# Kernel tuning notes

Measured on AMD Instinct MI355X. Metric: run time of the kernel, lower is better.

## Reference

```python
import jax, jax.numpy as jnp
import numpy as np

B, F, P, CIN, C, NH, HID, DEPTH = 32, 243, 17, 2, 128, 8, 256, 4
EPS = 1e-6


def setup_inputs() -> dict:
    key = jax.random.key(0)
    ks = jax.random.split(key, 9)
    s = jnp.float32(0.02)
    return {
        "x": jax.random.normal(ks[0], (B, F, P, CIN), jnp.float32),
        "adj": jax.random.uniform(ks[1], (P, P), jnp.float32),
        "w_embed": jax.random.normal(ks[2], (CIN, C), jnp.float32) * s,
        "b_embed": jnp.zeros((C,), jnp.float32),
        "pos": jax.random.normal(ks[3], (P, C), jnp.float32) * s,
        "ln1_g": jnp.ones((DEPTH, C), jnp.float32),
        "ln1_b": jnp.zeros((DEPTH, C), jnp.float32),
        "w_qkv": jax.random.normal(ks[4], (DEPTH, C, 3 * C), jnp.float32) * s,
        "b_qkv": jnp.zeros((DEPTH, 3 * C), jnp.float32),
        "w_gate": jax.random.normal(ks[5], (DEPTH, C), jnp.float32) * s,
        "b_gate": jnp.zeros((DEPTH,), jnp.float32),
        "w_proj": jax.random.normal(ks[6], (DEPTH, C, C), jnp.float32) * s,
        "b_proj": jnp.zeros((DEPTH, C), jnp.float32),
        "ln2_g": jnp.ones((DEPTH, C), jnp.float32),
        "ln2_b": jnp.zeros((DEPTH, C), jnp.float32),
        "w_fc1": jax.random.normal(ks[7], (DEPTH, C, HID), jnp.float32) * s,
        "b_fc1": jnp.zeros((DEPTH, HID), jnp.float32),
        "w_fc2": jax.random.normal(ks[8], (DEPTH, HID, C), jnp.float32) * s,
        "b_fc2": jnp.zeros((DEPTH, C), jnp.float32),
        "fn_g": jnp.ones((C,), jnp.float32),
        "fn_b": jnp.zeros((C,), jnp.float32),
    }


def _ln(x, g, b):
    m = x.mean(-1, keepdims=True)
    v = ((x - m) ** 2).mean(-1, keepdims=True)
    return (x - m) * jax.lax.rsqrt(v + EPS) * g + b


def reference(x, adj, w_embed, b_embed, pos, ln1_g, ln1_b, w_qkv, b_qkv,
              w_gate, b_gate, w_proj, b_proj, ln2_g, ln2_b,
              w_fc1, b_fc1, w_fc2, b_fc2, fn_g, fn_b):
    b, f, p, _ = x.shape
    hd = C // NH
    scale = jnp.float32(hd) ** -0.5
    # (b f p c) -> (b*f, p, c); joint-wise patch embedding + spatial pos embed
    h = x.reshape(b * f, p, -1) @ w_embed + b_embed + pos  # (BF, P, C)
    adj4 = adj[None, None]  # (1,1,P,P)
    for i in range(DEPTH):
        y = _ln(h, ln1_g[i], ln1_b[i])
        qkv = (y @ w_qkv[i] + b_qkv[i]).reshape(b * f, p, 3, NH, hd)
        q = qkv[:, :, 0].transpose(0, 2, 1, 3)  # (BF, NH, P, hd)
        k = qkv[:, :, 1].transpose(0, 2, 1, 3)
        v = qkv[:, :, 2].transpose(0, 2, 1, 3)
        attn = jnp.einsum('bhnd,bhmd->bhnm', q, k) * scale  # (BF, NH, P, P)
        # skeleton gate: Linear(dim,1)+sigmoid, broadcast over the key axis
        gate = jax.nn.sigmoid(y @ w_gate[i] + b_gate[i])  # (BF, P)
        gb = gate[:, None, None, :]  # (BF,1,1,P)
        attn = attn * (1.0 - gb) + adj4 * gb
        attn = jax.nn.softmax(attn, axis=-1)
        o = jnp.einsum('bhnm,bhmd->bhnd', attn, v)
        o = o.transpose(0, 2, 1, 3).reshape(b * f, p, C)
        h = h + o @ w_proj[i] + b_proj[i]
        y2 = _ln(h, ln2_g[i], ln2_b[i])
        h = h + jax.nn.gelu(y2 @ w_fc1[i] + b_fc1[i], approximate=False) @ w_fc2[i] + b_fc2[i]
    h = _ln(h, fn_g, fn_b)
    return h.reshape(b, f, p, C)
```

## Files before the change

kernel.cpp:

```cpp
#include <hip/hip_runtime.h>
#include <math.h>

#define DEPTH 4
#define C 128
#define P 17
#define HID 256
#define SPB 4
#define GR 34
#define ROWS 68
#define MT 3
#define LS 132
#define QS 136
#define SEGQ (ROWS*QS)
#define AS 264
#define ARENA_N (ROWS*AS)
#define NTHREADS 256

#define WTQ 0
#define WTP 196608
#define WT1 262144
#define WT2 393216
#define LO_OFF 524288

typedef short short8 __attribute__((ext_vector_type(8)));
typedef float f32x4 __attribute__((ext_vector_type(4)));

__device__ __forceinline__ unsigned short f2bf(float f) {
    unsigned int u = __float_as_uint(f);
    u += 0x7FFFu + ((u >> 16) & 1u);
    return (unsigned short)(u >> 16);
}
__device__ __forceinline__ float bf2f(unsigned short s) {
    return __uint_as_float((unsigned int)s << 16);
}
__device__ __forceinline__ void unpack8(uint4 u, float* f) {
    f[0] = __uint_as_float(u.x << 16); f[1] = __uint_as_float(u.x & 0xffff0000u);
    f[2] = __uint_as_float(u.y << 16); f[3] = __uint_as_float(u.y & 0xffff0000u);
    f[4] = __uint_as_float(u.z << 16); f[5] = __uint_as_float(u.z & 0xffff0000u);
    f[6] = __uint_as_float(u.w << 16); f[7] = __uint_as_float(u.w & 0xffff0000u);
}

extern "C" __global__ void prep_wt(const float* __restrict__ wq, const float* __restrict__ wp,
                                   const float* __restrict__ w1, const float* __restrict__ w2,
                                   unsigned short* __restrict__ ws) {
    int idx = blockIdx.x * 256 + threadIdx.x;
    int rel = idx; const float* W; int K, N;
    if (rel < 196608)                  { W = wq; K = 128; N = 384; }
    else if ((rel -= 196608) < 65536)  { W = wp; K = 128; N = 128; }
    else if ((rel -= 65536) < 131072)  { W = w1; K = 128; N = 256; }
    else { rel -= 131072;                W = w2; K = 256; N = 128; }
    int per = K * N;
    int l = rel / per, r = rel % per;
    int n = r / K, k = r % K;
    float wv = W[l * per + k * N + n];
    unsigned short h = f2bf(wv);
    ws[idx] = h;
    ws[idx + LO_OFF] = f2bf(wv - bf2f(h));
}

template<int NTW, int KS>
__device__ __forceinline__ void gemm_bt2(const unsigned short* A0, const unsigned short* A1,
        int astride, int aLoOff,
        const unsigned short* __restrict__ WT, int ldk, int ntoff, int ksoff,
        int wave, int lane, f32x4 (&acc0)[MT][NTW], f32x4 (&acc1)[MT][NTW])
{
    int m = lane & 15, q = lane >> 4;
    int arow[MT];
    #pragma unroll
    for (int mt = 0; mt < MT; ++mt) {
        int ar = mt * 16 + m;
        arow[mt] = (ar >= GR) ? (ar - 16) : ar;
    }
    for (int ks = 0; ks < KS; ++ks) {
        short8 ah0[MT], al0[MT], ah1[MT], al1[MT];
        #pragma unroll
        for (int mt = 0; mt < MT; ++mt) {
            int off = arow[mt] * astride + ks * 32 + q * 8;
            ah0[mt] = *(const short8*)&A0[off];
            al0[mt] = *(const short8*)&A0[off + aLoOff];
            ah1[mt] = *(const short8*)&A1[off];
            al1[mt] = *(const short8*)&A1[off + aLoOff];
        }
        #pragma unroll
        for (int nt = 0; nt < NTW; ++nt) {
            int nrow = (ntoff + wave * NTW + nt) * 16 + m;
            const unsigned short* bp = WT + nrow * ldk + (ksoff + ks) * 32 + q * 8;
            short8 bh = *(const short8*)bp;
            short8 bl = *(const short8*)(bp + LO_OFF);
            #pragma unroll
            for (int mt = 0; mt < MT; ++mt) {
                acc0[mt][nt] = __builtin_amdgcn_mfma_f32_16x16x32_bf16(ah0[mt], bh, acc0[mt][nt], 0, 0, 0);
                acc1[mt][nt] = __builtin_amdgcn_mfma_f32_16x16x32_bf16(ah1[mt], bh, acc1[mt][nt], 0, 0, 0);
                acc0[mt][nt] = __builtin_amdgcn_mfma_f32_16x16x32_bf16(al0[mt], bh, acc0[mt][nt], 0, 0, 0);
                acc1[mt][nt] = __builtin_amdgcn_mfma_f32_16x16x32_bf16(al1[mt], bh, acc1[mt][nt], 0, 0, 0);
                acc0[mt][nt] = __builtin_amdgcn_mfma_f32_16x16x32_bf16(ah0[mt], bl, acc0[mt][nt], 0, 0, 0);
                acc1[mt][nt] = __builtin_amdgcn_mfma_f32_16x16x32_bf16(ah1[mt], bl, acc1[mt][nt], 0, 0, 0);
            }
        }
    }
}

template<int NTW>
__device__ __forceinline__ void zero_acc(f32x4 (&acc)[MT][NTW]) {
    #pragma unroll
    for (int mt = 0; mt < MT; ++mt)
        #pragma unroll
        for (int nt = 0; nt < NTW; ++nt) acc[mt][nt] = (f32x4){0.f, 0.f, 0.f, 0.f};
}

template<int MODE>
__device__ __forceinline__ void ln_stage(const float* h_s, unsigned short* dst, float* gate_s,
        const float* __restrict__ g, const float* __restrict__ b,
        const float* __restrict__ wg, float bgate,
        float* __restrict__ outp, int tok0, int wave, int lane)
{
    int half = lane >> 5, l2 = lane & 31;
    #pragma unroll
    for (int it = 0; it < 9; ++it) {
        int row = it * 8 + wave * 2 + half;
        if (row < ROWS) {
            float4 v = *(const float4*)&h_s[row * LS + l2 * 4];
            float s  = v.x + v.y + v.z + v.w;
            float ss = v.x*v.x + v.y*v.y + v.z*v.z + v.w*v.w;
            #pragma unroll
            for (int o = 16; o > 0; o >>= 1) { s += __shfl_xor(s, o, 32); ss += __shfl_xor(ss, o, 32); }
            float mean = s * (1.f / C);
            float rstd = rsqrtf(ss * (1.f / C) - mean * mean + 1e-6f);
            float4 gg = *(const float4*)&g[l2 * 4];
            float4 bb = *(const float4*)&b[l2 * 4];
            float e0 = (v.x - mean) * rstd * gg.x + bb.x;
            float e1 = (v.y - mean) * rstd * gg.y + bb.y;
            float e2 = (v.z - mean) * rstd * gg.z + bb.z;
            float e3 = (v.w - mean) * rstd * gg.w + bb.w;
            if (MODE == 2) {
                *(float4*)&outp[(tok0 + row) * C + l2 * 4] = make_float4(e0, e1, e2, e3);
            } else {
                unsigned short h0 = f2bf(e0), h1 = f2bf(e1), h2 = f2bf(e2), h3 = f2bf(e3);
                *(ushort4*)&dst[row * AS + l2 * 4] = make_ushort4(h0, h1, h2, h3);
                *(ushort4*)&dst[row * AS + 128 + l2 * 4] =
                    make_ushort4(f2bf(e0 - bf2f(h0)), f2bf(e1 - bf2f(h1)),
                                 f2bf(e2 - bf2f(h2)), f2bf(e3 - bf2f(h3)));
                if (MODE == 0) {
                    float4 wv = *(const float4*)&wg[l2 * 4];
                    float gp = e0*wv.x + e1*wv.y + e2*wv.z + e3*wv.w;
                    #pragma unroll
                    for (int o = 16; o > 0; o >>= 1) gp += __shfl_xor(gp, o, 32);
                    if (l2 == 0) gate_s[row] = 1.f / (1.f + expf(-(gp + bgate)));
                }
            }
        }
    }
}

extern "C" __global__ __launch_bounds__(NTHREADS, 1)
void pose3d_r14(const float* __restrict__ x, const float* __restrict__ adj,
                 const float* __restrict__ w_embed, const float* __restrict__ b_embed,
                 const float* __restrict__ pos,
                 const float* __restrict__ ln1_g, const float* __restrict__ ln1_b,
                 const float* __restrict__ b_qkv,
                 const float* __restrict__ w_gate, const float* __restrict__ b_gate,
                 const float* __restrict__ b_proj,
                 const float* __restrict__ ln2_g, const float* __restrict__ ln2_b,
                 const float* __restrict__ b_fc1, const float* __restrict__ b_fc2,
                 const float* __restrict__ fn_g, const float* __restrict__ fn_b,
                 const unsigned short* __restrict__ wsw,
                 float* __restrict__ out)
{
    __shared__ __align__(16) float h_s[ROWS * LS];
    __shared__ __align__(16) unsigned short u_s[3 * SEGQ];
    __shared__ __align__(16) unsigned short arena[ARENA_N];
    __shared__ float adj_s[P * P];
    __shared__ float gate_s[ROWS];

    const int tid = threadIdx.x;
    const int wave = tid >> 6, lane = tid & 63;
    const int m16 = lane & 15, q4 = lane >> 4;
    const int blk = blockIdx.x;

    for (int idx = tid; idx < ROWS * C; idx += NTHREADS) {
        int row = idx >> 7, c = idx & 127;
        int s = row / 17, p = row % 17;
        int xb = (blk * SPB + s) * (P * 2) + p * 2;
        h_s[row * LS + c] = x[xb] * w_embed[c] + x[xb + 1] * w_embed[C + c]
                          + b_embed[c] + pos[p * C + c];
    }
    for (int idx = tid; idx < P * P; idx += NTHREADS) adj_s[idx] = adj[idx];
    __syncthreads();

    const unsigned short* const ar0 = arena;
    const unsigned short* const ar1 = arena + GR * AS;

    for (int i = 0; i < DEPTH; ++i) {
        ln_stage<0>(h_s, arena, gate_s, ln1_g + i * C, ln1_b + i * C,
                    w_gate + i * C, b_gate[i], nullptr, 0, wave, lane);
        __syncthreads();

        #pragma unroll
        for (int pass = 0; pass < 2; ++pass) {
            f32x4 acc0[MT][3], acc1[MT][3];
            zero_acc<3>(acc0); zero_acc<3>(acc1);
            gemm_bt2<3, 4>(ar0, ar1, AS, 128, wsw + WTQ + i * 49152, 128, pass * 12, 0,
                           wave, lane, acc0, acc1);
            const float* bq = b_qkv + i * 384;
            #pragma unroll
            for (int nt = 0; nt < 3; ++nt) {
                int n = (pass * 12 + wave * 3 + nt) * 16 + m16;
                float bias = bq[n];
                int t = n >> 7, cc = n & 127;
                #pragma unroll
                for (int mt = 0; mt < MT; ++mt)
                    #pragma unroll
                    for (int r = 0; r < 4; ++r) {
                        int row = mt * 16 + q4 * 4 + r;
                        if (row < GR) {
                            u_s[t * SEGQ + row * QS + cc]        = f2bf(acc0[mt][nt][r] + bias);
                            u_s[t * SEGQ + (GR + row) * QS + cc] = f2bf(acc1[mt][nt][r] + bias);
                        }
                    }
            }
        }
        __syncthreads();

        for (int task = tid; task < 544; task += NTHREADS) {
            int n = task >> 5, sh = task & 31;
            int s = sh >> 3, hh = sh & 7;
            int base = s * 17;
            float qv[16];
            { const uint4* qp = (const uint4*)&u_s[(base + n) * QS + hh * 16];
              unpack8(qp[0], qv); unpack8(qp[1], qv + 8); }
            float Sv[17]; float mx = -1e30f;
            #pragma unroll
            for (int mm = 0; mm < 17; ++mm) {
                const uint4* kp = (const uint4*)&u_s[SEGQ + (base + mm) * QS + hh * 16];
                float kf[16]; unpack8(kp[0], kf); unpack8(kp[1], kf + 8);
                float acc = 0.f;
                #pragma unroll
                for (int d = 0; d < 16; ++d) acc += qv[d] * kf[d];
                float gt = gate_s[base + mm];
                float aa = acc * 0.25f * (1.f - gt) + adj_s[n * P + mm] * gt;
                Sv[mm] = aa; mx = fmaxf(mx, aa);
            }
            float sum = 0.f;
            #pragma unroll
            for (int mm = 0; mm < 17; ++mm) { float e = expf(Sv[mm] - mx); Sv[mm] = e; sum += e; }
            float inv = 1.f / sum;
            float ov[16];
            #pragma unroll
            for (int d = 0; d < 16; ++d) ov[d] = 0.f;
            #pragma unroll
            for (int mm = 0; mm < 17; ++mm) {
                const uint4* vp = (const uint4*)&u_s[2 * SEGQ + (base + mm) * QS + hh * 16];
                float vf[16]; unpack8(vp[0], vf); unpack8(vp[1], vf + 8);
                float w = Sv[mm];
                #pragma unroll
                for (int d = 0; d < 16; ++d) ov[d] += w * vf[d];
            }
            short8 h0, h1, l0, l1;
            #pragma unroll
            for (int d = 0; d < 8; ++d) {
                float va = ov[d] * inv, vb = ov[d + 8] * inv;
                unsigned short ha = f2bf(va), hb = f2bf(vb);
                h0[d] = (short)ha; h1[d] = (short)hb;
                l0[d] = (short)f2bf(va - bf2f(ha));
                l1[d] = (short)f2bf(vb - bf2f(hb));
            }
            unsigned short* op = &arena[(base + n) * AS + hh * 16];
            *(short8*)&op[0]   = h0;
            *(short8*)&op[8]   = h1;
            *(short8*)&op[128] = l0;
            *(short8*)&op[136] = l1;
        }
        __syncthreads();

        {
            f32x4 acc0[MT][2], acc1[MT][2];
            zero_acc<2>(acc0); zero_acc<2>(acc1);
            gemm_bt2<2, 4>(ar0, ar1, AS, 128, wsw + WTP + i * 16384, 128, 0, 0,
                           wave, lane, acc0, acc1);
            const float* bp = b_proj + i * C;
            #pragma unroll
            for (int nt = 0; nt < 2; ++nt) {
                int n = (wave * 2 + nt) * 16 + m16;
                float bias = bp[n];
                #pragma unroll
                for (int mt = 0; mt < MT; ++mt)
                    #pragma unroll
                    for (int r = 0; r < 4; ++r) {
                        int row = mt * 16 + q4 * 4 + r;
                        if (row < GR) {
                            h_s[row * LS + n]        += acc0[mt][nt][r] + bias;
                            h_s[(GR + row) * LS + n] += acc1[mt][nt][r] + bias;
                        }
                    }
            }
        }
        __syncthreads();

        ln_stage<1>(h_s, arena, gate_s, ln2_g + i * C, ln2_b + i * C,
                    nullptr, 0.f, nullptr, 0, wave, lane);
        __syncthreads();

        {
            const unsigned short* const t0 = u_s;
            const unsigned short* const t1 = u_s + GR * AS;
            f32x4 acc20[MT][2], acc21[MT][2];
            zero_acc<2>(acc20); zero_acc<2>(acc21);
            for (int hf = 0; hf < 2; ++hf) {
                f32x4 acc10[MT][2], acc11[MT][2];
                zero_acc<2>(acc10); zero_acc<2>(acc11);
                gemm_bt2<2, 4>(ar0, ar1, AS, 128, wsw + WT1 + i * 32768, 128, hf * 8, 0,
                               wave, lane, acc10, acc11);
                const float* b1 = b_fc1 + i * HID + hf * 128;
                #pragma unroll
                for (int nt = 0; nt < 2; ++nt) {
                    int nl = (wave * 2 + nt) * 16 + m16;
                    float bias = b1[nl];
                    #pragma unroll
                    for (int mt = 0; mt < MT; ++mt)
                        #pragma unroll
                        for (int r = 0; r < 4; ++r) {
                            int row = mt * 16 + q4 * 4 + r;
                            if (row < GR) {
                                float xx = acc10[mt][nt][r] + bias;
                                float ge = 0.5f * xx * (1.f + erff(xx * 0.70710678118654752f));
                                unsigned short hb = f2bf(ge);
                                u_s[row * AS + nl] = hb;
                                u_s[row * AS + 128 + nl] = f2bf(ge - bf2f(hb));
                                float xx1 = acc11[mt][nt][r] + bias;
                                float ge1 = 0.5f * xx1 * (1.f + erff(xx1 * 0.70710678118654752f));
                                unsigned short hb1 = f2bf(ge1);
                                u_s[(GR + row) * AS + nl] = hb1;
                                u_s[(GR + row) * AS + 128 + nl] = f2bf(ge1 - bf2f(hb1));
                            }
                        }
                }
                __syncthreads();
                gemm_bt2<2, 4>(t0, t1, AS, 128, wsw + WT2 + i * 32768, 256, 0, hf * 4,
                               wave, lane, acc20, acc21);
                __syncthreads();
            }
            const float* b2 = b_fc2 + i * C;
            #pragma unroll
            for (int nt = 0; nt < 2; ++nt) {
                int n = (wave * 2 + nt) * 16 + m16;
                float bias = b2[n];
                #pragma unroll
                for (int mt = 0; mt < MT; ++mt)
                    #pragma unroll
                    for (int r = 0; r < 4; ++r) {
                        int row = mt * 16 + q4 * 4 + r;
                        if (row < GR) {
                            h_s[row * LS + n]        += acc20[mt][nt][r] + bias;
                            h_s[(GR + row) * LS + n] += acc21[mt][nt][r] + bias;
                        }
                    }
            }
        }
        __syncthreads();
    }

    ln_stage<2>(h_s, nullptr, nullptr, fn_g, fn_b, nullptr, 0.f, out, blk * ROWS, wave, lane);
}

extern "C" void kernel_launch(void* const* d_in, const int* in_sizes, int n_in,
                              void* d_out, int out_size, void* d_ws, size_t ws_size,
                              hipStream_t stream) {
    const float* x       = (const float*)d_in[0];
    const float* adj     = (const float*)d_in[1];
    const float* w_embed = (const float*)d_in[2];
    const float* b_embed = (const float*)d_in[3];
    const float* pos     = (const float*)d_in[4];
    const float* ln1_g   = (const float*)d_in[5];
    const float* ln1_b   = (const float*)d_in[6];
    const float* w_qkv   = (const float*)d_in[7];
    const float* b_qkv   = (const float*)d_in[8];
    const float* w_gate  = (const float*)d_in[9];
    const float* b_gate  = (const float*)d_in[10];
    const float* w_proj  = (const float*)d_in[11];
    const float* b_proj  = (const float*)d_in[12];
    const float* ln2_g   = (const float*)d_in[13];
    const float* ln2_b   = (const float*)d_in[14];
    const float* w_fc1   = (const float*)d_in[15];
    const float* b_fc1   = (const float*)d_in[16];
    const float* w_fc2   = (const float*)d_in[17];
    const float* b_fc2   = (const float*)d_in[18];
    const float* fn_g    = (const float*)d_in[19];
    const float* fn_b    = (const float*)d_in[20];
    unsigned short* ws   = (unsigned short*)d_ws;
    float* out = (float*)d_out;

    prep_wt<<<2048, 256, 0, stream>>>(w_qkv, w_proj, w_fc1, w_fc2, ws);
    pose3d_r14<<<1944, NTHREADS, 0, stream>>>(x, adj, w_embed, b_embed, pos,
        ln1_g, ln1_b, b_qkv, w_gate, b_gate, b_proj, ln2_g, ln2_b,
        b_fc1, b_fc2, fn_g, fn_b, ws, out);
}
```

Baseline: 1.882 ms.

## Pair query rows per attention thread and restructure MLP to cut barriers

Result: slower. 6.195 ms (+229.1%).

```diff
diff --git a/kernel.cpp b/kernel.cpp
--- a/kernel.cpp
+++ b/kernel.cpp
@@ -153,7 +153,7 @@
 }
 
 extern "C" __global__ __launch_bounds__(NTHREADS, 1)
-void pose3d_r14(const float* __restrict__ x, const float* __restrict__ adj,
+void pose3d_r15(const float* __restrict__ x, const float* __restrict__ adj,
                  const float* __restrict__ w_embed, const float* __restrict__ b_embed,
                  const float* __restrict__ pos,
                  const float* __restrict__ ln1_g, const float* __restrict__ ln1_b,
@@ -221,54 +221,85 @@
         }
         __syncthreads();
 
-        for (int task = tid; task < 544; task += NTHREADS) {
-            int n = task >> 5, sh = task & 31;
-            int s = sh >> 3, hh = sh & 7;
+        for (int u = tid; u < 288; u += NTHREADS) {
+            int s = u / 72, rr = u % 72, hh = rr / 9, g = rr % 9;
             int base = s * 17;
-            float qv[16];
-            { const uint4* qp = (const uint4*)&u_s[(base + n) * QS + hh * 16];
-              unpack8(qp[0], qv); unpack8(qp[1], qv + 8); }
-            float Sv[17]; float mx = -1e30f;
+            bool two = (g < 8);
+            int na = two ? g : 16;
+            int nb = two ? (g + 8) : 16;
+            float qa[16], qb[16];
+            { const uint4* qp = (const uint4*)&u_s[(base + na) * QS + hh * 16];
+              unpack8(qp[0], qa); unpack8(qp[1], qa + 8); }
+            { const uint4* qp = (const uint4*)&u_s[(base + nb) * QS + hh * 16];
+              unpack8(qp[0], qb); unpack8(qp[1], qb + 8); }
+            float Sa[17], Sb[17]; float mxa = -1e30f, mxb = -1e30f;
             #pragma unroll
             for (int mm = 0; mm < 17; ++mm) {
                 const uint4* kp = (const uint4*)&u_s[SEGQ + (base + mm) * QS + hh * 16];
                 float kf[16]; unpack8(kp[0], kf); unpack8(kp[1], kf + 8);
-                float acc = 0.f;
-                #pragma unroll
-                for (int d = 0; d < 16; ++d) acc += qv[d] * kf[d];
+                float a0 = 0.f, a1 = 0.f, b0 = 0.f, b1 = 0.f;
+                #pragma unroll
+                for (int d = 0; d < 16; d += 2) {
+                    a0 += qa[d] * kf[d];     a1 += qa[d+1] * kf[d+1];
+                    b0 += qb[d] * kf[d];     b1 += qb[d+1] * kf[d+1];
+                }
                 float gt = gate_s[base + mm];
-                float aa = acc * 0.25f * (1.f - gt) + adj_s[n * P + mm] * gt;
-                Sv[mm] = aa; mx = fmaxf(mx, aa);
-            }
-            float sum = 0.f;
-            #pragma unroll
-            for (int mm = 0; mm < 17; ++mm) { float e = expf(Sv[mm] - mx); Sv[mm] = e; sum += e; }
-            float inv = 1.f / sum;
-            float ov[16];
-            #pragma unroll
-            for (int d = 0; d < 16; ++d) ov[d] = 0.f;
+                float sc = 0.25f * (1.f - gt);
+                float aa = (a0 + a1) * sc + adj_s[na * P + mm] * gt;
+                float ab = (b0 + b1) * sc + adj_s[nb * P + mm] * gt;
+                Sa[mm] = aa; mxa = fmaxf(mxa, aa);
+                Sb[mm] = ab; mxb = fmaxf(mxb, ab);
+            }
+            float suma = 0.f, sumb = 0.f;
+            #pragma unroll
+            for (int mm = 0; mm < 17; ++mm) {
+                float ea = expf(Sa[mm] - mxa); Sa[mm] = ea; suma += ea;
+                float eb = expf(Sb[mm] - mxb); Sb[mm] = eb; sumb += eb;
+            }
+            float inva = 1.f / suma, invb = 1.f / sumb;
+            float ova[16], ovb[16];
+            #pragma unroll
+            for (int d = 0; d < 16; ++d) { ova[d] = 0.f; ovb[d] = 0.f; }
             #pragma unroll
             for (int mm = 0; mm < 17; ++mm) {
                 const uint4* vp = (const uint4*)&u_s[2 * SEGQ + (base + mm) * QS + hh * 16];
                 float vf[16]; unpack8(vp[0], vf); unpack8(vp[1], vf + 8);
-                float w = Sv[mm];
-                #pragma unroll
-                for (int d = 0; d < 16; ++d) ov[d] += w * vf[d];
-            }
-            short8 h0, h1, l0, l1;
-            #pragma unroll
-            for (int d = 0; d < 8; ++d) {
-                float va = ov[d] * inv, vb = ov[d + 8] * inv;
-                unsigned short ha = f2bf(va), hb = f2bf(vb);
-                h0[d] = (short)ha; h1[d] = (short)hb;
-                l0[d] = (short)f2bf(va - bf2f(ha));
-                l1[d] = (short)f2bf(vb - bf2f(hb));
-            }
-            unsigned short* op = &arena[(base + n) * AS + hh * 16];
-            *(short8*)&op[0]   = h0;
-            *(short8*)&op[8]   = h1;
-            *(short8*)&op[128] = l0;
-            *(short8*)&op[136] = l1;
+                float wa = Sa[mm], wb = Sb[mm];
+                #pragma unroll
+                for (int d = 0; d < 16; ++d) { ova[d] += wa * vf[d]; ovb[d] += wb * vf[d]; }
+            }
+            {
+                short8 h0, h1, l0, l1;
+                #pragma unroll
+                for (int d = 0; d < 8; ++d) {
+                    float va = ova[d] * inva, vb2 = ova[d + 8] * inva;
+                    unsigned short ha = f2bf(va), hb = f2bf(vb2);
+                    h0[d] = (short)ha; h1[d] = (short)hb;
+                    l0[d] = (short)f2bf(va - bf2f(ha));
+                    l1[d] = (short)f2bf(vb2 - bf2f(hb));
+                }
+                unsigned short* op = &arena[(base + na) * AS + hh * 16];
+                *(short8*)&op[0]   = h0;
+                *(short8*)&op[8]   = h1;
+                *(short8*)&op[128] = l0;
+                *(short8*)&op[136] = l1;
+            }
+            if (two) {
+                short8 h0, h1, l0, l1;
+                #pragma unroll
+                for (int d = 0; d < 8; ++d) {
+                    float va = ovb[d] * invb, vb2 = ovb[d + 8] * invb;
+                    unsigned short ha = f2bf(va), hb = f2bf(vb2);
+                    h0[d] = (short)ha; h1[d] = (short)hb;
+                    l0[d] = (short)f2bf(va - bf2f(ha));
+                    l1[d] = (short)f2bf(vb2 - bf2f(hb));
+                }
+                unsigned short* op = &arena[(base + nb) * AS + hh * 16];
+                *(short8*)&op[0]   = h0;
+                *(short8*)&op[8]   = h1;
+                *(short8*)&op[128] = l0;
+                *(short8*)&op[136] = l1;
+            }
         }
         __syncthreads();
 
@@ -301,32 +332,28 @@
         __syncthreads();
 
         {
-            const unsigned short* const t0 = u_s;
-            const unsigned short* const t1 = u_s + GR * AS;
-            f32x4 acc20[MT][2], acc21[MT][2];
-            zero_acc<2>(acc20); zero_acc<2>(acc21);
-            for (int hf = 0; hf < 2; ++hf) {
-                f32x4 acc10[MT][2], acc11[MT][2];
-                zero_acc<2>(acc10); zero_acc<2>(acc11);
-                gemm_bt2<2, 4>(ar0, ar1, AS, 128, wsw + WT1 + i * 32768, 128, hf * 8, 0,
-                               wave, lane, acc10, acc11);
-                const float* b1 = b_fc1 + i * HID + hf * 128;
+            const float* b1v = b_fc1 + i * HID;
+            {
+                f32x4 a10[MT][2], a11[MT][2];
+                zero_acc<2>(a10); zero_acc<2>(a11);
+                gemm_bt2<2, 4>(ar0, ar1, AS, 128, wsw + WT1 + i * 32768, 128, 0, 0,
+                               wave, lane, a10, a11);
                 #pragma unroll
                 for (int nt = 0; nt < 2; ++nt) {
                     int nl = (wave * 2 + nt) * 16 + m16;
-                    float bias = b1[nl];
+                    float bias = b1v[nl];
                     #pragma unroll
                     for (int mt = 0; mt < MT; ++mt)
                         #pragma unroll
                         for (int r = 0; r < 4; ++r) {
                             int row = mt * 16 + q4 * 4 + r;
                             if (row < GR) {
-                                float xx = acc10[mt][nt][r] + bias;
+                                float xx = a10[mt][nt][r] + bias;
                                 float ge = 0.5f * xx * (1.f + erff(xx * 0.70710678118654752f));
                                 unsigned short hb = f2bf(ge);
                                 u_s[row * AS + nl] = hb;
                                 u_s[row * AS + 128 + nl] = f2bf(ge - bf2f(hb));
-                                float xx1 = acc11[mt][nt][r] + bias;
+                                float xx1 = a11[mt][nt][r] + bias;
                                 float ge1 = 0.5f * xx1 * (1.f + erff(xx1 * 0.70710678118654752f));
                                 unsigned short hb1 = f2bf(ge1);
                                 u_s[(GR + row) * AS + nl] = hb1;
@@ -334,11 +361,45 @@
                             }
                         }
                 }
+            }
+            {
+                f32x4 a10[MT][2], a11[MT][2];
+                zero_acc<2>(a10); zero_acc<2>(a11);
+                gemm_bt2<2, 4>(ar0, ar1, AS, 128, wsw + WT1 + i * 32768, 128, 8, 0,
+                               wave, lane, a10, a11);
                 __syncthreads();
-                gemm_bt2<2, 4>(t0, t1, AS, 128, wsw + WT2 + i * 32768, 256, 0, hf * 4,
-                               wave, lane, acc20, acc21);
-                __syncthreads();
-            }
+                #pragma unroll
+                for (int nt = 0; nt < 2; ++nt) {
+                    int nl = (wave * 2 + nt) * 16 + m16;
+                    float bias = b1v[128 + nl];
+                    #pragma unroll
+                    for (int mt = 0; mt < MT; ++mt)
+                        #pragma unroll
+                        for (int r = 0; r < 4; ++r) {
+                            int row = mt * 16 + q4 * 4 + r;
+                            if (row < GR) {
+                                float xx = a10[mt][nt][r] + bias;
+                                float ge = 0.5f * xx * (1.f + erff(xx * 0.70710678118654752f));
+                                unsigned short hb = f2bf(ge);
+                                arena[row * AS + nl] = hb;
+                                arena[row * AS + 128 + nl] = f2bf(ge - bf2f(hb));
+                                float xx1 = a11[mt][nt][r] + bias;
+                                float ge1 = 0.5f * xx1 * (1.f + erff(xx1 * 0.70710678118654752f));
+                                unsigned short hb1 = f2bf(ge1);
+                                arena[(GR + row) * AS + nl] = hb1;
+                                arena[(GR + row) * AS + 128 + nl] = f2bf(ge1 - bf2f(hb1));
+                            }
+                        }
+                }
+            }
+            __syncthreads();
+
+            f32x4 acc20[MT][2], acc21[MT][2];
+            zero_acc<2>(acc20); zero_acc<2>(acc21);
+            gemm_bt2<2, 4>(u_s, u_s + GR * AS, AS, 128, wsw + WT2 + i * 32768, 256, 0, 0,
+                           wave, lane, acc20, acc21);
+            gemm_bt2<2, 4>(ar0, ar1, AS, 128, wsw + WT2 + i * 32768, 256, 0, 4,
+                           wave, lane, acc20, acc21);
             const float* b2 = b_fc2 + i * C;
             #pragma unroll
             for (int nt = 0; nt < 2; ++nt) {
@@ -390,7 +451,7 @@
     float* out = (float*)d_out;
 
     prep_wt<<<2048, 256, 0, stream>>>(w_qkv, w_proj, w_fc1, w_fc2, ws);
-    pose3d_r14<<<1944, NTHREADS, 0, stream>>>(x, adj, w_embed, b_embed, pos,
+    pose3d_r15<<<1944, NTHREADS, 0, stream>>>(x, adj, w_embed, b_embed, pos,
         ln1_g, ln1_b, b_qkv, w_gate, b_gate, b_proj, ln2_g, ln2_b,
         b_fc1, b_fc2, fn_g, fn_b, ws, out);
 }
```
